# Kernel tuning notes

Hardware: AMD Instinct MI355X
Metric: run time of the kernel (lower is better)

The kernel has to match this reference:

```python
import jax, jax.numpy as jnp
import numpy as np

B, S = 2, 2048
Q_DIM, KV_DIM = 2048, 2048
N_HEADS, HEAD_DIM = 16, 128
N_KV_HEADS = 4            # kv_bandwidth 512 // head_dim 128
N_REP = N_HEADS // N_KV_HEADS
EPS = 1e-5


def setup_inputs() -> dict:
    key = jax.random.key(0)
    ks = jax.random.split(key, 6)
    return {
        "q_stream": jax.random.normal(ks[0], (B, S, Q_DIM), jnp.float32),
        "kv_stream": jax.random.normal(ks[1], (B, S, KV_DIM), jnp.float32),
        "wq": jax.random.normal(ks[2], (Q_DIM, N_HEADS * HEAD_DIM), jnp.float32) * 0.02,
        "wk": jax.random.normal(ks[3], (KV_DIM, N_KV_HEADS * HEAD_DIM), jnp.float32) * 0.02,
        "wv": jax.random.normal(ks[4], (KV_DIM, N_KV_HEADS * HEAD_DIM), jnp.float32) * 0.02,
        "wo": jax.random.normal(ks[5], (N_HEADS * HEAD_DIM, Q_DIM), jnp.float32) * 0.02,
        "q_norm_w": jnp.ones((HEAD_DIM,), jnp.float32),
        "k_norm_w": jnp.ones((HEAD_DIM,), jnp.float32),
    }


def _rmsnorm(x, w):
    # RMSNorm over the last (head_dim) axis
    var = jnp.mean(x * x, axis=-1, keepdims=True)
    return x * jax.lax.rsqrt(var + EPS) * w


def reference(q_stream, kv_stream, wq, wk, wv, wo, q_norm_w, k_norm_w):
    b, s, _ = q_stream.shape
    # QKV projections (weights stored [in, out])
    xq = jnp.einsum("bsd,de->bse", q_stream, wq).reshape(b, s, N_HEADS, HEAD_DIM)
    xk = jnp.einsum("bsd,de->bse", kv_stream, wk).reshape(b, s, N_KV_HEADS, HEAD_DIM)
    xv = jnp.einsum("bsd,de->bse", kv_stream, wv).reshape(b, s, N_KV_HEADS, HEAD_DIM)
    # qk_norm_mode == "before_rope": per-head RMSNorm on q and k
    xq = _rmsnorm(xq, q_norm_w)
    xk = _rmsnorm(xk, k_norm_w)
    # GQA: repeat kv heads to match query heads
    k = jnp.repeat(xk, N_REP, axis=2)  # [b, s, H, D]
    v = jnp.repeat(xv, N_REP, axis=2)
    # causal scaled-dot-product attention
    scale = 1.0 / np.sqrt(HEAD_DIM).astype(np.float32)
    scores = jnp.einsum("bqhd,bkhd->bhqk", xq, k) * scale  # [b, H, S, S]
    causal = jnp.tril(jnp.ones((s, s), dtype=bool))
    scores = jnp.where(causal, scores, jnp.finfo(scores.dtype).min)
    probs = jax.nn.softmax(scores, axis=-1)
    out = jnp.einsum("bhqk,bkhd->bqhd", probs, v).reshape(b, s, N_HEADS * HEAD_DIM)
    return jnp.einsum("bse,eo->bso", out, wo)
```

## Files before the change

### kernel.cpp

```cpp
#include <hip/hip_runtime.h>
#include <cstdint>


using bf16 = __bf16;
using bf16x4 = __attribute__((ext_vector_type(4))) __bf16;
using bf16x8 = __attribute__((ext_vector_type(8))) __bf16;
using s16x4  = __attribute__((ext_vector_type(4))) short;
using f32x4  = __attribute__((ext_vector_type(4))) float;

#define SEQ 2048
#define NH 16
#define NKVH 4
#define HD 128

#define NEG (-3.0e38f)

#if defined(__has_builtin)
#if __has_builtin(__builtin_amdgcn_mfma_f32_16x16x16bf16_1k)
#define HAVE_1K 1
#endif
#endif
__device__ __forceinline__ f32x4 mfma_16x16x16(bf16x4 a, bf16x4 b, f32x4 c) {
#ifdef HAVE_1K
    return __builtin_amdgcn_mfma_f32_16x16x16bf16_1k(
        __builtin_bit_cast(s16x4, a), __builtin_bit_cast(s16x4, b), c, 0, 0, 0);
#else
    f32x4 d;
    asm volatile("v_mfma_f32_16x16x16_bf16 %0, %1, %2, %3"
                 : "=v"(d) : "v"(a), "v"(b), "v"(c));
    return d;
#endif
}

__device__ __forceinline__ float fast_exp2(float x) {
#if defined(__has_builtin)
#if __has_builtin(__builtin_amdgcn_exp2f)
    return __builtin_amdgcn_exp2f(x);
#else
    return exp2f(x);
#endif
#else
    return exp2f(x);
#endif
}

__device__ __forceinline__ void load_lds16(const bf16* g, bf16* l) {
    __builtin_amdgcn_global_load_lds(
        (const __attribute__((address_space(1))) unsigned int*)g,
        (__attribute__((address_space(3))) unsigned int*)l, 16, 0, 0);
}

__global__ __launch_bounds__(256) void cvt_both(const float* __restrict__ q,
                                                const float* __restrict__ kv,
                                                bf16* __restrict__ oq,
                                                bf16* __restrict__ okv) {
    int i = blockIdx.x * 256 + threadIdx.x;
    const float* in;
    bf16* out;
    int j;
    if (i < 1048576) { in = q;  out = oq;  j = i; }
    else             { in = kv; out = okv; j = i - 1048576; }
    const float4* p = (const float4*)in + (long)j * 2;
    float4 f0 = p[0], f1 = p[1];
    bf16x8 o = {(bf16)f0.x, (bf16)f0.y, (bf16)f0.z, (bf16)f0.w,
                (bf16)f1.x, (bf16)f1.y, (bf16)f1.z, (bf16)f1.w};
    *((bf16x8*)out + j) = o;
}

__device__ __forceinline__ void transpose_body(const float* in, bf16* out,
                                               int R, int C, int bx, int by) {
    __shared__ bf16 tile[32][33];
    int x  = bx * 32 + threadIdx.x;
    int y0 = by * 32 + threadIdx.y;
#pragma unroll
    for (int i = 0; i < 32; i += 8) {
        int y = y0 + i;
        if (y < R && x < C) tile[threadIdx.y + i][threadIdx.x] = (bf16)in[(long)y * C + x];
    }
    __syncthreads();
    int ox  = by * 32 + threadIdx.x;
    int oy0 = bx * 32 + threadIdx.y;
#pragma unroll
    for (int i = 0; i < 32; i += 8) {
        int oy = oy0 + i;
        if (oy < C && ox < R) out[(long)oy * R + ox] = tile[threadIdx.x][threadIdx.y + i];
    }
}

__global__ void transpose2d(const float* __restrict__ in, bf16* __restrict__ out,
                            int R, int C) {
    transpose_body(in, out, R, C, blockIdx.x, blockIdx.y);
}

__global__ void transpose_merged(const float* __restrict__ wq,
                                 const float* __restrict__ wk,
                                 const float* __restrict__ wv,
                                 bf16* __restrict__ wqT,
                                 bf16* __restrict__ wkvT) {
    if (blockIdx.z == 0) {
        transpose_body(wq, wqT, 2048, 2048, blockIdx.x, blockIdx.y);
    } else {
        int x = blockIdx.x;
        if (x >= 32) return;
        if (x < 16) transpose_body(wk, wkvT, 2048, 512, x, blockIdx.y);
        else        transpose_body(wv, wkvT + 512L * 2048, 2048, 512, x - 16, blockIdx.y);
    }
}

template <typename CT>
__device__ __forceinline__ void gemm_block(const bf16* A, const bf16* BT, CT* C,
                                           int N, int K, int m0, int n0,
                                           bf16 (*As)[128][32], bf16 (*Bs)[128][32]) {
    const int tid  = threadIdx.x;
    const int wave = tid >> 6, lane = tid & 63;
    const int wm = (wave >> 1) * 64, wn = (wave & 1) * 64;
    const int lrow = lane & 15, quad = lane >> 4;
    const int lko = quad * 8;

    const bf16* ga0 = A  + (long)(m0 + (tid >> 2)) * K + (tid & 3) * 8;
    const bf16* ga1 = ga0 + 64L * K;
    const bf16* gb0 = BT + (long)(n0 + (tid >> 2)) * K + (tid & 3) * 8;
    const bf16* gb1 = gb0 + 64L * K;
    bf16* la0 = &As[0][0][0] + tid * 8;
    bf16* lb0 = &Bs[0][0][0] + tid * 8;

    f32x4 acc[4][4] = {};

    const int nIt = K >> 5;
    load_lds16(ga0, la0);
    load_lds16(ga1, la0 + 2048);
    load_lds16(gb0, lb0);
    load_lds16(gb1, lb0 + 2048);
    __syncthreads();

#pragma unroll 1
    for (int it = 0; it < nIt; ++it) {
        const int cur = it & 1;
        if (it + 1 < nIt) {
            const int k0 = (it + 1) * 32;
            bf16* la = la0 + (cur ^ 1) * 4096;
            bf16* lb = lb0 + (cur ^ 1) * 4096;
            load_lds16(ga0 + k0, la);
            load_lds16(ga1 + k0, la + 2048);
            load_lds16(gb0 + k0, lb);
            load_lds16(gb1 + k0, lb + 2048);
        }
        bf16x8 af[4], bfr[4];
#pragma unroll
        for (int i = 0; i < 4; ++i) af[i]  = *(const bf16x8*)(&As[cur][wm + i * 16 + lrow][lko]);
#pragma unroll
        for (int j = 0; j < 4; ++j) bfr[j] = *(const bf16x8*)(&Bs[cur][wn + j * 16 + lrow][lko]);
#pragma unroll
        for (int i = 0; i < 4; ++i)
#pragma unroll
            for (int j = 0; j < 4; ++j)
                acc[i][j] = __builtin_amdgcn_mfma_f32_16x16x32_bf16(af[i], bfr[j], acc[i][j], 0, 0, 0);
        __syncthreads();
    }
#pragma unroll
    for (int i = 0; i < 4; ++i) {
        int mrow0 = m0 + wm + i * 16 + quad * 4;
#pragma unroll
        for (int j = 0; j < 4; ++j) {
            int ncol = n0 + wn + j * 16 + lrow;
#pragma unroll
            for (int r = 0; r < 4; ++r)
                C[(long)(mrow0 + r) * N + ncol] = (CT)acc[i][j][r];
        }
    }
}

template <typename CT>
__global__ __launch_bounds__(256) void gemm_bt(const bf16* __restrict__ A,
                                               const bf16* __restrict__ BT,
                                               CT* __restrict__ C,
                                               int M, int N, int K) {
    __shared__ bf16 As[2][128][32];
    __shared__ bf16 Bs[2][128][32];
    const int nwg = gridDim.x * gridDim.y;
    const int bid = blockIdx.y * gridDim.x + blockIdx.x;
    const int swz = (bid & 7) * (nwg >> 3) + (bid >> 3);
    const int bx = swz % gridDim.x, by = swz / gridDim.x;
    gemm_block<CT>(A, BT, C, N, K, by * 128, bx * 128, As, Bs);
}

__global__ __launch_bounds__(256) void gemm12(const bf16* __restrict__ A1,
                                              const bf16* __restrict__ B1,
                                              bf16* __restrict__ C1,
                                              const bf16* __restrict__ A2,
                                              const bf16* __restrict__ B2,
                                              bf16* __restrict__ C2) {
    __shared__ bf16 As[2][128][32];
    __shared__ bf16 Bs[2][128][32];
    const int bid = blockIdx.x;
    const bf16 *A, *BT;
    bf16* C;
    int N, gx, sub, nsub;
    if (bid < 512) { A = A1; BT = B1; C = C1; N = 2048; gx = 16; sub = bid;       nsub = 512; }
    else           { A = A2; BT = B2; C = C2; N = 1024; gx = 8;  sub = bid - 512; nsub = 256; }
    const int swz = (sub & 7) * (nsub >> 3) + (sub >> 3);
    const int bx = swz % gx, by = swz / gx;
    gemm_block<bf16>(A, BT, C, N, 2048, by * 128, bx * 128, As, Bs);
}

__global__ __launch_bounds__(256) void rmsnorm_merged(bf16* __restrict__ XQ,
                                                      bf16* __restrict__ XKV,
                                                      const float* __restrict__ QW,
                                                      const float* __restrict__ KW) {
    int v = blockIdx.x * 4 + (threadIdx.x >> 6);
    int lane = threadIdx.x & 63;
    bf16* X; const float* W; int lhpr, stride, vv;
    if (v < 65536) { X = XQ;  W = QW; lhpr = 4; stride = 2048; vv = v; }
    else           { X = XKV; W = KW; lhpr = 2; stride = 1024; vv = v - 65536; }
    int row = vv >> lhpr, head = vv & ((1 << lhpr) - 1);
    bf16* x = X + (long)row * stride + head * HD;
    float fa = (float)x[lane * 2], fb = (float)x[lane * 2 + 1];
    float ss = fa * fa + fb * fb;
#pragma unroll
    for (int off = 1; off < 64; off <<= 1) ss += __shfl_xor(ss, off, 64);
    float r = rsqrtf(ss * (1.0f / 128.0f) + 1e-5f);
    x[lane * 2]     = (bf16)(fa * r * W[lane * 2]);
    x[lane * 2 + 1] = (bf16)(fb * r * W[lane * 2 + 1]);
}

__global__ __launch_bounds__(256) void repack_merged(const bf16* __restrict__ xkv,
                                                     bf16* __restrict__ kf,
                                                     bf16* __restrict__ vf) {
    __shared__ bf16 Vls[64][136];
    int kt = blockIdx.x, kvh = blockIdx.y, b = blockIdx.z;
    int tid = threadIdx.x, lane = tid & 63;
    int lrow = lane & 15, quad = lane >> 4;

    {
        int ks = tid >> 6;
        const bf16* src = xkv + ((long)b * SEQ + kt * 64) * 1024 + kvh * HD;
        bf16* dst = kf + ((long)((b * NKVH + kvh) * 32 + kt)) * 8192;
#pragma unroll
        for (int nt = 0; nt < 4; ++nt) {
            bf16x8 v = *(const bf16x8*)(src + (long)(nt * 16 + lrow) * 1024 + ks * 32 + quad * 8);
            *(bf16x8*)(dst + ((nt * 4 + ks) * 64 + lane) * 8) = v;
        }
    }

    {
        const bf16* src = xkv + ((long)b * SEQ + kt * 64) * 1024 + 512 + kvh * HD;
#pragma unroll
        for (int p = 0; p < 4; ++p) {
            int c = p * 256 + tid;
            int r = c >> 4, dc = (c & 15) * 8;
            *(uint4*)(&Vls[r][dc]) = *(const uint4*)(src + (long)r * 1024 + dc);
        }
        __syncthreads();
        int w = tid >> 6;
        bf16* dst = vf + ((long)((b * NKVH + kvh) * 32 + kt)) * 8192;
#pragma unroll
        for (int nt = 0; nt < 4; ++nt)
#pragma unroll
            for (int dtl = 0; dtl < 2; ++dtl) {
                int dt = w * 2 + dtl;
                bf16x4 v = {Vls[nt * 16 + quad * 4 + 0][dt * 16 + lrow],
                            Vls[nt * 16 + quad * 4 + 1][dt * 16 + lrow],
                            Vls[nt * 16 + quad * 4 + 2][dt * 16 + lrow],
                            Vls[nt * 16 + quad * 4 + 3][dt * 16 + lrow]};
                *(bf16x4*)(dst + ((nt * 8 + dt) * 64 + lane) * 4) = v;
            }
    }
}

__global__ __launch_bounds__(512, 4) void attn_kernel(const bf16* __restrict__ Q,
                                                      const bf16* __restrict__ KF,
                                                      const bf16* __restrict__ VF,
                                                      bf16* __restrict__ O) {
    __shared__ bf16 Kf[2][8192];
    __shared__ bf16 Vf[2][8192];
    const int tid = threadIdx.x, wave = tid >> 6, lane = tid & 63;
    const int w4 = wave & 3, grpW = wave >> 2;
    const int bid = blockIdx.x;
    const int grp = bid & 7;
    const int b = grp >> 2, kvh = grp & 3;
    const int slot = bid >> 3;
    const int pr = slot & 15;
    const int h = kvh * 4 + (slot >> 4);
    const int lrow = lane & 15, quad = lane >> 4;
    const float scl2 = 0.12751744f;
    const float THR = 62.7f;

    const int qt1 = 31 - pr, qt2 = pr;

    const bf16* kfb = KF + ((long)(b * NKVH + kvh) * 32) * 8192;
    const bf16* vfb = VF + ((long)(b * NKVH + kvh) * 32) * 8192;

    auto stage = [&](int pair, int bsel) {
        const bf16* kg = kfb + (long)pair * 8192 + tid * 8;
        const bf16* vg = vfb + (long)pair * 8192 + tid * 8;
        bf16* kd = &Kf[bsel][0] + tid * 8;
        bf16* vd = &Vf[bsel][0] + tid * 8;
        load_lds16(kg, kd);
        load_lds16(kg + 4096, kd + 4096);
        load_lds16(vg, vd);
        load_lds16(vg + 4096, vd + 4096);
    };

    float m_i = NEG, l_i = 0.f;
    f32x4 oT[8] = {};
    bf16x8 bqw[4];

    auto combine_write_reset = [&](int qrow) {
        float a1keep = 0.f;
        float* vs = (float*)&Vf[0][0];
        const int sl = w4 * 64 + lane;
        __syncthreads();
        if (grpW == 1) {
            float* d = vs + sl * 18;
#pragma unroll
            for (int dt = 0; dt < 4; ++dt)
#pragma unroll
                for (int r = 0; r < 4; ++r) d[dt * 4 + r] = oT[dt][r];
            d[16] = m_i; d[17] = l_i;
        }
        __syncthreads();
        if (grpW == 0) {
            const float* s = vs + sl * 18;
            float m1 = s[16], l1 = s[17];
            float ms = fmaxf(m_i, m1);
            float a0 = fast_exp2((m_i - ms) * scl2);
            float a1 = fast_exp2((m1 - ms) * scl2);
            a1keep = a1;
            l_i = a0 * l_i + a1 * l1;
#pragma unroll
            for (int dt = 0; dt < 4; ++dt)
#pragma unroll
                for (int r = 0; r < 4; ++r)
                    oT[dt][r] = a0 * oT[dt][r] + a1 * s[dt * 4 + r];
#pragma unroll
            for (int dt = 4; dt < 8; ++dt)
#pragma unroll
                for (int r = 0; r < 4; ++r) oT[dt][r] *= a0;
            m_i = ms;
        }
        __syncthreads();
        if (grpW == 1) {
            float* d = vs + sl * 16;
#pragma unroll
            for (int dt = 4; dt < 8; ++dt)
#pragma unroll
                for (int r = 0; r < 4; ++r) d[(dt - 4) * 4 + r] = oT[dt][r];
        }
        __syncthreads();
        if (grpW == 0) {
            const float* s = vs + sl * 16;
#pragma unroll
            for (int dt = 4; dt < 8; ++dt)
#pragma unroll
                for (int r = 0; r < 4; ++r) oT[dt][r] += a1keep * s[(dt - 4) * 4 + r];
            float inv_l = 1.0f / l_i;
            bf16* obase = O + ((long)(b * SEQ + qrow)) * (NH * HD) + h * HD;
#pragma unroll
            for (int dt = 0; dt < 8; ++dt) {
                bf16x4 o = {(bf16)(oT[dt][0] * inv_l), (bf16)(oT[dt][1] * inv_l),
                            (bf16)(oT[dt][2] * inv_l), (bf16)(oT[dt][3] * inv_l)};
                *(bf16x4*)(obase + dt * 16 + quad * 4) = o;
            }
        }
        __syncthreads();
        m_i = NEG; l_i = 0.f;
#pragma unroll
        for (int dt = 0; dt < 8; ++dt)
#pragma unroll
            for (int r = 0; r < 4; ++r) oT[dt][r] = 0.f;
    };

    auto process = [&](int i, int itN, int myq, int cur) {
        const int kbg = 2 * i + grpW;
        const bool diag = (i == itN - 1);
        const bf16* kbase = &Kf[cur][0] + grpW * 4096;
        const bf16* vbase = &Vf[cur][0] + grpW * 4096;

        f32x4 st[2];
        __builtin_amdgcn_s_setprio(1);
#pragma unroll
        for (int nt = 0; nt < 2; ++nt) {
            f32x4 acc = {};
#pragma unroll
            for (int ks = 0; ks < 4; ++ks) {
                bf16x8 ak = *(const bf16x8*)(kbase + (nt * 4 + ks) * 512 + lane * 8);
                acc = __builtin_amdgcn_mfma_f32_16x16x32_bf16(ak, bqw[ks], acc, 0, 0, 0);
            }
            st[nt] = acc;
        }
        __builtin_amdgcn_s_setprio(0);
        if (diag) {
#pragma unroll
            for (int nt = 0; nt < 2; ++nt) {
                int kp0 = kbg * 32 + nt * 16 + quad * 4;
#pragma unroll
                for (int r = 0; r < 4; ++r)
                    if (kp0 + r > myq) st[nt][r] = NEG;
            }
        }

        float mx = st[0][0];
#pragma unroll
        for (int nt = 0; nt < 2; ++nt)
#pragma unroll
            for (int r = 0; r < 4; ++r) mx = fmaxf(mx, st[nt][r]);
        mx = fmaxf(mx, __shfl_xor(mx, 16, 64));
        mx = fmaxf(mx, __shfl_xor(mx, 32, 64));

        if (!__all(mx - m_i <= THR)) {
            float mnew = fmaxf(m_i, mx);
            float alpha = fast_exp2((m_i - mnew) * scl2);
            l_i *= alpha;
#pragma unroll
            for (int dt = 0; dt < 8; ++dt)
#pragma unroll
                for (int r = 0; r < 4; ++r) oT[dt][r] *= alpha;
            m_i = mnew;
        }
        float rs = 0.f;
#pragma unroll
        for (int nt = 0; nt < 2; ++nt)
#pragma unroll
            for (int r = 0; r < 4; ++r) {
                float p = fast_exp2((st[nt][r] - m_i) * scl2);
                st[nt][r] = p;
                rs += p;
            }
        rs += __shfl_xor(rs, 16, 64);
        rs += __shfl_xor(rs, 32, 64);
        l_i += rs;

        bf16x4 pf[2];
#pragma unroll
        for (int nt = 0; nt < 2; ++nt) {
            bf16x4 tt = {(bf16)st[nt][0], (bf16)st[nt][1],
                         (bf16)st[nt][2], (bf16)st[nt][3]};
            pf[nt] = tt;
        }

        __builtin_amdgcn_s_setprio(1);
#pragma unroll
        for (int nt = 0; nt < 2; ++nt)
#pragma unroll
            for (int dt = 0; dt < 8; ++dt) {
                bf16x4 av = *(const bf16x4*)(vbase + (nt * 8 + dt) * 256 + lane * 4);
                oT[dt] = mfma_16x16x16(av, pf[nt], oT[dt]);
            }
        __builtin_amdgcn_s_setprio(0);
    };

    const int it1 = qt1 + 1;
    const int myq1 = qt1 * 64 + w4 * 16 + lrow;
    {
        const bf16* qrow = Q + ((long)(b * SEQ + myq1)) * (NH * HD) + h * HD;
#pragma unroll
        for (int ks = 0; ks < 4; ++ks)
            bqw[ks] = *(const bf16x8*)(qrow + ks * 32 + quad * 8);
    }
    stage(0, 0);
    __syncthreads();
#pragma unroll 1
    for (int i = 0; i < it1; ++i) {
        const int cur = i & 1;
        if (i + 1 < it1) stage(i + 1, cur ^ 1);
        process(i, it1, myq1, cur);
        __syncthreads();
    }
    combine_write_reset(myq1);

    const int it2 = qt2 + 1;
    const int myq2 = qt2 * 64 + w4 * 16 + lrow;
    {
        const bf16* qrow = Q + ((long)(b * SEQ + myq2)) * (NH * HD) + h * HD;
#pragma unroll
        for (int ks = 0; ks < 4; ++ks)
            bqw[ks] = *(const bf16x8*)(qrow + ks * 32 + quad * 8);
    }
    stage(0, 0);
    __syncthreads();
#pragma unroll 1
    for (int i = 0; i < it2; ++i) {
        const int cur = i & 1;
        if (i + 1 < it2) stage(i + 1, cur ^ 1);
        process(i, it2, myq2, cur);
        __syncthreads();
    }
    combine_write_reset(myq2);
}

extern "C" void kernel_launch(void* const* d_in, const int* in_sizes, int n_in,
                              void* d_out, int out_size, void* d_ws, size_t ws_size,
                              hipStream_t stream) {
    const float* q_stream  = (const float*)d_in[0];
    const float* kv_stream = (const float*)d_in[1];
    const float* wq  = (const float*)d_in[2];
    const float* wk  = (const float*)d_in[3];
    const float* wv  = (const float*)d_in[4];
    const float* wo  = (const float*)d_in[5];
    const float* qnw = (const float*)d_in[6];
    const float* knw = (const float*)d_in[7];
    float* out = (float*)d_out;

    bf16* ws   = (bf16*)d_ws;
    bf16* sb   = ws;
    bf16* wqT  = ws + 8L * 1024 * 1024;
    bf16* wkvT = wqT + 4L * 1024 * 1024;
    bf16* xq   = wkvT + 2L * 1024 * 1024;
    bf16* xkv  = xq + 8L * 1024 * 1024;
    bf16* kf   = xkv + 4L * 1024 * 1024;
    bf16* vf   = kf + 2L * 1024 * 1024;
    bf16* sbKV = (bf16*)d_out;

    dim3 tb(32, 8);
    cvt_both<<<8192, 256, 0, stream>>>(q_stream, kv_stream, sb, sbKV);
    transpose_merged<<<dim3(64, 64, 2), tb, 0, stream>>>(wq, wk, wv, wqT, wkvT);
    gemm12<<<768, 256, 0, stream>>>(sb, wqT, xq, sbKV, wkvT, xkv);
    transpose2d<<<dim3(64, 64), tb, 0, stream>>>(wo, wqT, 2048, 2048);
    rmsnorm_merged<<<20480, 256, 0, stream>>>(xq, xkv, qnw, knw);
    repack_merged<<<dim3(32, 4, 2), 256, 0, stream>>>(xkv, kf, vf);
    attn_kernel<<<dim3(512), dim3(512), 0, stream>>>(xq, kf, vf, sb);
    gemm_bt<float><<<dim3(16, 32), 256, 0, stream>>>(sb, wqT, out, 4096, 2048, 2048);

    (void)in_sizes; (void)n_in; (void)out_size; (void)ws_size;
}
```

Before: 352.8 us.

## Fuse RMSNorm into QKV GEMM epilogue and merge prep kernels

Folds the per-head q/k RMSNorm into the QKV projection GEMM epilogue. Each 128-wide N tile is exactly one head, so the sum of squares is reduced across the two N-waves through LDS. This removes a separate read-modify-write pass over xq and xk. It also merges input conversion with the weight transposes, and the wo transpose with the K/V repack, into single launches. Together these cut the launch count from eight to five, at the cost of an extra barrier and shuffles in the GEMM tail and more branching per block.

```diff
diff --git a/kernel.cpp b/kernel.cpp
--- a/kernel.cpp
+++ b/kernel.cpp
@@ -50,67 +50,66 @@
         (__attribute__((address_space(3))) unsigned int*)l, 16, 0, 0);
 }
 
-__global__ __launch_bounds__(256) void cvt_both(const float* __restrict__ q,
-                                                const float* __restrict__ kv,
-                                                bf16* __restrict__ oq,
-                                                bf16* __restrict__ okv) {
-    int i = blockIdx.x * 256 + threadIdx.x;
-    const float* in;
-    bf16* out;
-    int j;
-    if (i < 1048576) { in = q;  out = oq;  j = i; }
-    else             { in = kv; out = okv; j = i - 1048576; }
-    const float4* p = (const float4*)in + (long)j * 2;
-    float4 f0 = p[0], f1 = p[1];
-    bf16x8 o = {(bf16)f0.x, (bf16)f0.y, (bf16)f0.z, (bf16)f0.w,
-                (bf16)f1.x, (bf16)f1.y, (bf16)f1.z, (bf16)f1.w};
-    *((bf16x8*)out + j) = o;
-}
-
-__device__ __forceinline__ void transpose_body(const float* in, bf16* out,
+__device__ __forceinline__ void transpose_flat(const float* in, bf16* out,
                                                int R, int C, int bx, int by) {
     __shared__ bf16 tile[32][33];
-    int x  = bx * 32 + threadIdx.x;
-    int y0 = by * 32 + threadIdx.y;
+    int tx = threadIdx.x & 31, ty = threadIdx.x >> 5;
+    int x  = bx * 32 + tx;
+    int y0 = by * 32 + ty;
 #pragma unroll
     for (int i = 0; i < 32; i += 8) {
         int y = y0 + i;
-        if (y < R && x < C) tile[threadIdx.y + i][threadIdx.x] = (bf16)in[(long)y * C + x];
+        if (y < R && x < C) tile[ty + i][tx] = (bf16)in[(long)y * C + x];
     }
     __syncthreads();
-    int ox  = by * 32 + threadIdx.x;
-    int oy0 = bx * 32 + threadIdx.y;
+    int ox  = by * 32 + tx;
+    int oy0 = bx * 32 + ty;
 #pragma unroll
     for (int i = 0; i < 32; i += 8) {
         int oy = oy0 + i;
-        if (oy < C && ox < R) out[(long)oy * R + ox] = tile[threadIdx.x][threadIdx.y + i];
-    }
-}
-
-__global__ void transpose2d(const float* __restrict__ in, bf16* __restrict__ out,
-                            int R, int C) {
-    transpose_body(in, out, R, C, blockIdx.x, blockIdx.y);
-}
-
-__global__ void transpose_merged(const float* __restrict__ wq,
-                                 const float* __restrict__ wk,
-                                 const float* __restrict__ wv,
-                                 bf16* __restrict__ wqT,
-                                 bf16* __restrict__ wkvT) {
-    if (blockIdx.z == 0) {
-        transpose_body(wq, wqT, 2048, 2048, blockIdx.x, blockIdx.y);
+        if (oy < C && ox < R) out[(long)oy * R + ox] = tile[tx][ty + i];
+    }
+}
+
+__global__ __launch_bounds__(256) void cvt_trans(const float* __restrict__ q,
+                                                 const float* __restrict__ kv,
+                                                 bf16* __restrict__ oq,
+                                                 bf16* __restrict__ okv,
+                                                 const float* __restrict__ wq,
+                                                 const float* __restrict__ wk,
+                                                 const float* __restrict__ wv,
+                                                 bf16* __restrict__ wqT,
+                                                 bf16* __restrict__ wkvT) {
+    int bid = blockIdx.x;
+    if (bid < 8192) {
+        int i = bid * 256 + threadIdx.x;
+        const float* in;
+        bf16* out;
+        int j;
+        if (i < 1048576) { in = q;  out = oq;  j = i; }
+        else             { in = kv; out = okv; j = i - 1048576; }
+        const float4* p = (const float4*)in + (long)j * 2;
+        float4 f0 = p[0], f1 = p[1];
+        bf16x8 o = {(bf16)f0.x, (bf16)f0.y, (bf16)f0.z, (bf16)f0.w,
+                    (bf16)f1.x, (bf16)f1.y, (bf16)f1.z, (bf16)f1.w};
+        *((bf16x8*)out + j) = o;
+    } else if (bid < 12288) {
+        int t = bid - 8192;
+        transpose_flat(wq, wqT, 2048, 2048, t & 63, t >> 6);
+    } else if (bid < 13312) {
+        int t = bid - 12288;
+        transpose_flat(wk, wkvT, 2048, 512, t & 15, t >> 4);
     } else {
-        int x = blockIdx.x;
-        if (x >= 32) return;
-        if (x < 16) transpose_body(wk, wkvT, 2048, 512, x, blockIdx.y);
-        else        transpose_body(wv, wkvT + 512L * 2048, 2048, 512, x - 16, blockIdx.y);
-    }
-}
-
-template <typename CT>
+        int t = bid - 13312;
+        transpose_flat(wv, wkvT + 512L * 2048, 2048, 512, t & 15, t >> 4);
+    }
+}
+
+template <typename CT, bool NORM>
 __device__ __forceinline__ void gemm_block(const bf16* A, const bf16* BT, CT* C,
                                            int N, int K, int m0, int n0,
-                                           bf16 (*As)[128][32], bf16 (*Bs)[128][32]) {
+                                           bf16 (*As)[128][32], bf16 (*Bs)[128][32],
+                                           const float* Wn) {
     const int tid  = threadIdx.x;
     const int wave = tid >> 6, lane = tid & 63;
     const int wm = (wave >> 1) * 64, wn = (wave & 1) * 64;
@@ -157,6 +156,39 @@
                 acc[i][j] = __builtin_amdgcn_mfma_f32_16x16x32_bf16(af[i], bfr[j], acc[i][j], 0, 0, 0);
         __syncthreads();
     }
+
+    if constexpr (NORM) {
+        float* ssb = (float*)&As[0][0][0];
+#pragma unroll
+        for (int i = 0; i < 4; ++i)
+#pragma unroll
+            for (int r = 0; r < 4; ++r) {
+                float p = 0.f;
+#pragma unroll
+                for (int j = 0; j < 4; ++j) p += acc[i][j][r] * acc[i][j][r];
+                p += __shfl_xor(p, 1, 64);
+                p += __shfl_xor(p, 2, 64);
+                p += __shfl_xor(p, 4, 64);
+                p += __shfl_xor(p, 8, 64);
+                if (lrow == 0) ssb[(wave & 1) * 128 + wm + i * 16 + quad * 4 + r] = p;
+            }
+        __syncthreads();
+        float wgt[4];
+#pragma unroll
+        for (int j = 0; j < 4; ++j) wgt[j] = Wn[wn + j * 16 + lrow];
+#pragma unroll
+        for (int i = 0; i < 4; ++i) {
+            const int row0 = wm + i * 16 + quad * 4;
+#pragma unroll
+            for (int r = 0; r < 4; ++r) {
+                float tot = ssb[row0 + r] + ssb[128 + row0 + r];
+                float rsc = rsqrtf(tot * (1.0f / 128.0f) + 1e-5f);
+#pragma unroll
+                for (int j = 0; j < 4; ++j) acc[i][j][r] *= rsc * wgt[j];
+            }
+        }
+    }
+
 #pragma unroll
     for (int i = 0; i < 4; ++i) {
         int mrow0 = m0 + wm + i * 16 + quad * 4;
@@ -181,7 +213,7 @@
     const int bid = blockIdx.y * gridDim.x + blockIdx.x;
     const int swz = (bid & 7) * (nwg >> 3) + (bid >> 3);
     const int bx = swz % gridDim.x, by = swz / gridDim.x;
-    gemm_block<CT>(A, BT, C, N, K, by * 128, bx * 128, As, Bs);
+    gemm_block<CT, false>(A, BT, C, N, K, by * 128, bx * 128, As, Bs, nullptr);
 }
 
 __global__ __launch_bounds__(256) void gemm12(const bf16* __restrict__ A1,
@@ -189,45 +221,41 @@
                                               bf16* __restrict__ C1,
                                               const bf16* __restrict__ A2,
                                               const bf16* __restrict__ B2,
-                                              bf16* __restrict__ C2) {
+                                              bf16* __restrict__ C2,
+                                              const float* __restrict__ qnw,
+                                              const float* __restrict__ knw) {
     __shared__ bf16 As[2][128][32];
     __shared__ bf16 Bs[2][128][32];
     const int bid = blockIdx.x;
-    const bf16 *A, *BT;
-    bf16* C;
-    int N, gx, sub, nsub;
-    if (bid < 512) { A = A1; BT = B1; C = C1; N = 2048; gx = 16; sub = bid;       nsub = 512; }
-    else           { A = A2; BT = B2; C = C2; N = 1024; gx = 8;  sub = bid - 512; nsub = 256; }
-    const int swz = (sub & 7) * (nsub >> 3) + (sub >> 3);
-    const int bx = swz % gx, by = swz / gx;
-    gemm_block<bf16>(A, BT, C, N, 2048, by * 128, bx * 128, As, Bs);
-}
-
-__global__ __launch_bounds__(256) void rmsnorm_merged(bf16* __restrict__ XQ,
-                                                      bf16* __restrict__ XKV,
-                                                      const float* __restrict__ QW,
-                                                      const float* __restrict__ KW) {
-    int v = blockIdx.x * 4 + (threadIdx.x >> 6);
-    int lane = threadIdx.x & 63;
-    bf16* X; const float* W; int lhpr, stride, vv;
-    if (v < 65536) { X = XQ;  W = QW; lhpr = 4; stride = 2048; vv = v; }
-    else           { X = XKV; W = KW; lhpr = 2; stride = 1024; vv = v - 65536; }
-    int row = vv >> lhpr, head = vv & ((1 << lhpr) - 1);
-    bf16* x = X + (long)row * stride + head * HD;
-    float fa = (float)x[lane * 2], fb = (float)x[lane * 2 + 1];
-    float ss = fa * fa + fb * fb;
-#pragma unroll
-    for (int off = 1; off < 64; off <<= 1) ss += __shfl_xor(ss, off, 64);
-    float r = rsqrtf(ss * (1.0f / 128.0f) + 1e-5f);
-    x[lane * 2]     = (bf16)(fa * r * W[lane * 2]);
-    x[lane * 2 + 1] = (bf16)(fb * r * W[lane * 2 + 1]);
-}
-
-__global__ __launch_bounds__(256) void repack_merged(const bf16* __restrict__ xkv,
-                                                     bf16* __restrict__ kf,
-                                                     bf16* __restrict__ vf) {
+    if (bid < 512) {
+        const int swz = (bid & 7) * 64 + (bid >> 3);
+        const int bx = swz % 16, by = swz / 16;
+        gemm_block<bf16, true>(A1, B1, C1, 2048, 2048, by * 128, bx * 128, As, Bs, qnw);
+    } else {
+        const int sub = bid - 512;
+        const int swz = (sub & 7) * 32 + (sub >> 3);
+        const int bx = swz % 8, by = swz / 8;
+        const int n0 = bx * 128;
+        if (n0 < 512)
+            gemm_block<bf16, true>(A2, B2, C2, 1024, 2048, by * 128, n0, As, Bs, knw);
+        else
+            gemm_block<bf16, false>(A2, B2, C2, 1024, 2048, by * 128, n0, As, Bs, nullptr);
+    }
+}
+
+__global__ __launch_bounds__(256) void post_merged(const float* __restrict__ wo,
+                                                   bf16* __restrict__ woT,
+                                                   const bf16* __restrict__ xkv,
+                                                   bf16* __restrict__ kf,
+                                                   bf16* __restrict__ vf) {
     __shared__ bf16 Vls[64][136];
-    int kt = blockIdx.x, kvh = blockIdx.y, b = blockIdx.z;
+    int bid = blockIdx.x;
+    if (bid < 4096) {
+        transpose_flat(wo, woT, 2048, 2048, bid & 63, bid >> 6);
+        return;
+    }
+    int rb = bid - 4096;
+    int kt = rb & 31, kvh = (rb >> 5) & 3, b = rb >> 7;
     int tid = threadIdx.x, lane = tid & 63;
     int lrow = lane & 15, quad = lane >> 4;
 
@@ -511,13 +539,10 @@
     bf16* vf   = kf + 2L * 1024 * 1024;
     bf16* sbKV = (bf16*)d_out;
 
-    dim3 tb(32, 8);
-    cvt_both<<<8192, 256, 0, stream>>>(q_stream, kv_stream, sb, sbKV);
-    transpose_merged<<<dim3(64, 64, 2), tb, 0, stream>>>(wq, wk, wv, wqT, wkvT);
-    gemm12<<<768, 256, 0, stream>>>(sb, wqT, xq, sbKV, wkvT, xkv);
-    transpose2d<<<dim3(64, 64), tb, 0, stream>>>(wo, wqT, 2048, 2048);
-    rmsnorm_merged<<<20480, 256, 0, stream>>>(xq, xkv, qnw, knw);
-    repack_merged<<<dim3(32, 4, 2), 256, 0, stream>>>(xkv, kf, vf);
+    cvt_trans<<<14336, 256, 0, stream>>>(q_stream, kv_stream, sb, sbKV,
+                                         wq, wk, wv, wqT, wkvT);
+    gemm12<<<768, 256, 0, stream>>>(sb, wqT, xq, sbKV, wkvT, xkv, qnw, knw);
+    post_merged<<<4352, 256, 0, stream>>>(wo, wqT, xkv, kf, vf);
     attn_kernel<<<dim3(512), dim3(512), 0, stream>>>(xq, kf, vf, sb);
     gemm_bt<float><<<dim3(16, 32), 256, 0, stream>>>(sb, wqT, out, 4096, 2048, 2048);
 
```

Measured after the change: 330.0 us. 6.5% less time.
